# Kernel optimization log

Measured on AMD Instinct MI355X. Metric: run time of the kernel, lower is better.

Reference implementation:

```python
import jax, jax.numpy as jnp
import numpy as np

N = 50000
E = 1600000
EP = 500000
D_IN, D_EMB = 64, 32


def setup_inputs() -> dict:
    key = jax.random.key(0)
    ks = jax.random.split(key, 12)
    return {
        "x": jax.random.normal(ks[0], (N, D_IN), dtype=jnp.float32),
        "W1": jax.random.normal(ks[1], (D_IN, D_EMB), dtype=jnp.float32) * (1.0 / np.sqrt(D_IN)),
        "b1": jnp.zeros((D_EMB,), dtype=jnp.float32),
        "W2": jax.random.normal(ks[2], (D_EMB, 2 * D_EMB), dtype=jnp.float32) * (1.0 / np.sqrt(D_EMB)),
        "b2": jnp.zeros((2 * D_EMB,), dtype=jnp.float32),
        "eps": jax.random.normal(ks[3], (N, D_EMB), dtype=jnp.float32),
        "edge_src": jax.random.randint(ks[4], (E,), 0, N, dtype=jnp.int32),
        "edge_dst": jax.random.randint(ks[5], (E,), 0, N, dtype=jnp.int32),
        "pos_src": jax.random.randint(ks[6], (EP,), 0, N, dtype=jnp.int32),
        "pos_dst": jax.random.randint(ks[7], (EP,), 0, N, dtype=jnp.int32),
        "neg_src": jax.random.randint(ks[8], (EP,), 0, N, dtype=jnp.int32),
        "neg_dst": jax.random.randint(ks[9], (EP,), 0, N, dtype=jnp.int32),
    }


def _degree_norms(src, dst, n):
    ones = jnp.ones(src.shape, dtype=jnp.float32)
    out_deg = jax.ops.segment_sum(ones, src, num_segments=n)
    in_deg = jax.ops.segment_sum(ones, dst, num_segments=n)
    # DGL GraphConv norm='both': clamp degrees to >=1, pow(-0.5)
    return jnp.clip(out_deg, 1.0) ** -0.5, jnp.clip(in_deg, 1.0) ** -0.5


def _graph_conv(h, src, dst, norm_src, norm_dst, W, b, n):
    # rst = D_dst^{-1/2} A D_src^{-1/2} h W + b
    msg = (h * norm_src[:, None])[src]                       # [E, d] gather
    agg = jax.ops.segment_sum(msg, dst, num_segments=n)      # [N, d] scatter-add
    return (agg * norm_dst[:, None]) @ W + b


def _dot_predict(z, u, v):
    # u_dot_v: per-edge inner product of endpoint embeddings
    return jnp.sum(z[u] * z[v], axis=-1)


def reference(x, W1, b1, W2, b2, eps, edge_src, edge_dst,
              pos_src, pos_dst, neg_src, neg_dst):
    n = x.shape[0]
    ns, nd = _degree_norms(edge_src, edge_dst, n)
    h = _graph_conv(x, edge_src, edge_dst, ns, nd, W1, b1, n)
    h = jax.nn.relu(h)  # dropout = identity (eval mode)
    h = _graph_conv(h, edge_src, edge_dst, ns, nd, W2, b2, n)
    mu, log_var = jnp.split(h, 2, axis=-1)
    sigma = jnp.exp(log_var / 2.0)
    z = mu + sigma * eps
    pos = _dot_predict(z, pos_src, pos_dst)
    neg = _dot_predict(z, neg_src, neg_dst)
    return pos, neg, mu, sigma
```

## Files before the change

kernel.cpp:

```cpp
#include <hip/hip_runtime.h>
#include <math.h>

#define NN  50000
#define NE  1600000
#define NEP 500000
#define DIN 64
#define DE  32

#define BKT_SH 7
#define NB     391
#define S1B    250
#define CHK    6400
#define HB     128
#define HCHK   12500
#define HWRD   12500
#define XWB    3125

typedef float f4 __attribute__((ext_vector_type(4)));

__device__ __forceinline__ unsigned f2b(float f) {
    unsigned u = __float_as_uint(f);
    return (u + 0x7FFFu + ((u >> 16) & 1u)) >> 16;
}
__device__ __forceinline__ unsigned pack2(float a, float b) {
    return f2b(a) | (f2b(b) << 16);
}
__device__ __forceinline__ float blo(unsigned u) { return __uint_as_float(u << 16); }
__device__ __forceinline__ float bhi(unsigned u) { return __uint_as_float(u & 0xFFFF0000u); }

__global__ __launch_bounds__(256) void k_h1s1(const int* __restrict__ src,
                                              const int* __restrict__ dst,
                                              unsigned* __restrict__ partial,
                                              int* __restrict__ T) {
    __shared__ unsigned h[HWRD];
    int t = threadIdx.x;
    if (blockIdx.x < HB) {
        for (int i = t; i < HWRD; i += 256) h[i] = 0;
        __syncthreads();
        int beg = blockIdx.x * HCHK;
        const int ev = beg + HCHK;
        int i = beg + t;
        for (; i + 1792 < ev; i += 2048) {
            int s0 = src[i],        s1 = src[i + 256],  s2 = src[i + 512],  s3 = src[i + 768];
            int s4 = src[i + 1024], s5 = src[i + 1280], s6 = src[i + 1536], s7 = src[i + 1792];
            atomicAdd(&h[s0 >> 2], 1u << ((s0 & 3) * 8));
            atomicAdd(&h[s1 >> 2], 1u << ((s1 & 3) * 8));
            atomicAdd(&h[s2 >> 2], 1u << ((s2 & 3) * 8));
            atomicAdd(&h[s3 >> 2], 1u << ((s3 & 3) * 8));
            atomicAdd(&h[s4 >> 2], 1u << ((s4 & 3) * 8));
            atomicAdd(&h[s5 >> 2], 1u << ((s5 & 3) * 8));
            atomicAdd(&h[s6 >> 2], 1u << ((s6 & 3) * 8));
            atomicAdd(&h[s7 >> 2], 1u << ((s7 & 3) * 8));
        }
        for (; i < ev; i += 256) {
            int s = src[i];
            atomicAdd(&h[s >> 2], 1u << ((s & 3) * 8));
        }
        __syncthreads();
        unsigned* p = partial + (size_t)blockIdx.x * HWRD;
        for (int i2 = t; i2 < HWRD; i2 += 256) p[i2] = h[i2];
    } else {
        int b = blockIdx.x - HB;
        int* cd = (int*)h;
        for (int i = t; i < NB; i += 256) cd[i] = 0;
        __syncthreads();
        int beg = b * CHK;
        const int ev = beg + CHK;
        int i = beg + t;
        for (; i + 1792 < ev; i += 2048) {
            int d0 = dst[i],        d1 = dst[i + 256],  d2 = dst[i + 512],  d3 = dst[i + 768];
            int d4 = dst[i + 1024], d5 = dst[i + 1280], d6 = dst[i + 1536], d7 = dst[i + 1792];
            atomicAdd(&cd[d0 >> BKT_SH], 1);
            atomicAdd(&cd[d1 >> BKT_SH], 1);
            atomicAdd(&cd[d2 >> BKT_SH], 1);
            atomicAdd(&cd[d3 >> BKT_SH], 1);
            atomicAdd(&cd[d4 >> BKT_SH], 1);
            atomicAdd(&cd[d5 >> BKT_SH], 1);
            atomicAdd(&cd[d6 >> BKT_SH], 1);
            atomicAdd(&cd[d7 >> BKT_SH], 1);
        }
        for (; i < ev; i += 256)
            atomicAdd(&cd[dst[i] >> BKT_SH], 1);
        __syncthreads();
        for (int i2 = t; i2 < NB; i2 += 256) T[b * NB + i2] = cd[i2];
    }
}

__global__ __launch_bounds__(512) void k_s2h(const int* __restrict__ T,
                                             int* __restrict__ Base,
                                             int* __restrict__ BS,
                                             const unsigned* __restrict__ partial,
                                             int* __restrict__ degs) {
    int t = threadIdx.x;
    if (blockIdx.x == 0) {
        __shared__ int tot[512];
        int run = 0;
        if (t < NB) {
            for (int b = 0; b < S1B; b += 5) {
                int v0 = T[(b + 0) * NB + t];
                int v1 = T[(b + 1) * NB + t];
                int v2 = T[(b + 2) * NB + t];
                int v3 = T[(b + 3) * NB + t];
                int v4 = T[(b + 4) * NB + t];
                Base[(b + 0) * NB + t] = run; run += v0;
                Base[(b + 1) * NB + t] = run; run += v1;
                Base[(b + 2) * NB + t] = run; run += v2;
                Base[(b + 3) * NB + t] = run; run += v3;
                Base[(b + 4) * NB + t] = run; run += v4;
            }
        }
        tot[t] = (t < NB) ? run : 0;
        __syncthreads();
        for (int off = 1; off < 512; off <<= 1) {
            int v = (t >= off) ? tot[t - off] : 0;
            __syncthreads();
            tot[t] += v;
            __syncthreads();
        }
        if (t < NB) BS[t] = (t == 0) ? 0 : tot[t - 1];
        if (t == 0) BS[NB] = NE;
    } else {
        int w = (blockIdx.x - 1) * 512 + t;
        if (w < HWRD) {
            int c0 = 0, c1 = 0, c2 = 0, c3 = 0;
#pragma unroll 8
            for (int b = 0; b < HB; b++) {
                unsigned v = partial[(size_t)b * HWRD + w];
                c0 += (int)(v & 0xFFu);
                c1 += (int)((v >> 8) & 0xFFu);
                c2 += (int)((v >> 16) & 0xFFu);
                c3 += (int)(v >> 24);
            }
            ((int4*)degs)[w] = make_int4(c0, c1, c2, c3);
        }
    }
}

__global__ __launch_bounds__(512) void k_s3(const int* __restrict__ src,
                                            const int* __restrict__ dst,
                                            const int* __restrict__ T,
                                            const int* __restrict__ Base,
                                            const int* __restrict__ BS,
                                            unsigned* __restrict__ tmp) {
    __shared__ int scn[512];
    __shared__ int delta[NB];
    __shared__ int cur[NB];
    __shared__ unsigned buf[CHK];
    int t = threadIdx.x;
    int beg = blockIdx.x * CHK;
    scn[t] = (t < NB) ? T[blockIdx.x * NB + t] : 0;
    __syncthreads();
    for (int off = 1; off < 512; off <<= 1) {
        int v = (t >= off) ? scn[t - off] : 0;
        __syncthreads();
        scn[t] += v;
        __syncthreads();
    }
    if (t < NB) {
        int ls = (t == 0) ? 0 : scn[t - 1];
        cur[t] = ls;
        delta[t] = Base[blockIdx.x * NB + t] + BS[t] - ls;
    }
    __syncthreads();
    {
        const int ev = beg + CHK;
        int i = beg + t;
        for (; i + 1536 < ev; i += 2048) {
            int d0 = dst[i],        s0 = src[i];
            int d1 = dst[i + 512],  s1 = src[i + 512];
            int d2 = dst[i + 1024], s2 = src[i + 1024];
            int d3 = dst[i + 1536], s3 = src[i + 1536];
            int l0 = atomicAdd(&cur[d0 >> BKT_SH], 1); buf[l0] = (unsigned)s0 | ((unsigned)d0 << 16);
            int l1 = atomicAdd(&cur[d1 >> BKT_SH], 1); buf[l1] = (unsigned)s1 | ((unsigned)d1 << 16);
            int l2 = atomicAdd(&cur[d2 >> BKT_SH], 1); buf[l2] = (unsigned)s2 | ((unsigned)d2 << 16);
            int l3 = atomicAdd(&cur[d3 >> BKT_SH], 1); buf[l3] = (unsigned)s3 | ((unsigned)d3 << 16);
        }
        for (; i < ev; i += 512) {
            int d = dst[i];
            int s = src[i];
            int lp = atomicAdd(&cur[d >> BKT_SH], 1);
            buf[lp] = (unsigned)s | ((unsigned)d << 16);
        }
    }
    __syncthreads();
    for (int i = t; i < CHK; i += 512) {
        unsigned e = buf[i];
        tmp[delta[e >> (16 + BKT_SH)] + i] = e;
    }
}

__global__ __launch_bounds__(256) void k_s4x(const unsigned* __restrict__ tmp,
                                             const int* __restrict__ BS,
                                             ushort* __restrict__ csr,
                                             int* __restrict__ rowptr,
                                             const float* __restrict__ x,
                                             const float* __restrict__ W1,
                                             const int* __restrict__ degs,
                                             unsigned* __restrict__ xw1b) {
    __shared__ float sW[DIN * DE];
    int t = threadIdx.x;
    if (blockIdx.x < NB) {
        int* cnt = (int*)sW;
        int* scn = cnt + 128;
        int* cur = cnt + 256;
        int p = blockIdx.x;
        int ebeg = BS[p], eend = BS[p + 1];
        int ne = eend - ebeg;
        if (t < 128) cnt[t] = 0;
        __syncthreads();
        {
            int i = t;
            for (; i + 768 < ne; i += 1024) {
                unsigned e0 = tmp[ebeg + i];
                unsigned e1 = tmp[ebeg + i + 256];
                unsigned e2 = tmp[ebeg + i + 512];
                unsigned e3 = tmp[ebeg + i + 768];
                atomicAdd(&cnt[(e0 >> 16) & 127], 1);
                atomicAdd(&cnt[(e1 >> 16) & 127], 1);
                atomicAdd(&cnt[(e2 >> 16) & 127], 1);
                atomicAdd(&cnt[(e3 >> 16) & 127], 1);
            }
            for (; i < ne; i += 256)
                atomicAdd(&cnt[(tmp[ebeg + i] >> 16) & 127], 1);
        }
        __syncthreads();
        if (t < 128) scn[t] = cnt[t];
        __syncthreads();
        for (int off = 1; off < 128; off <<= 1) {
            int v = 0;
            if (t < 128 && t >= off) v = scn[t - off];
            __syncthreads();
            if (t < 128) scn[t] += v;
            __syncthreads();
        }
        if (t < 128) {
            int ex = (t == 0) ? 0 : scn[t - 1];
            cur[t] = ex;
            int node = (p << BKT_SH) + t;
            if (node < NN) rowptr[node] = ebeg + ex;
        }
        if (p == NB - 1 && t == 0) rowptr[NN] = NE;
        __syncthreads();
        {
            int i = t;
            for (; i + 768 < ne; i += 1024) {
                unsigned e0 = tmp[ebeg + i];
                unsigned e1 = tmp[ebeg + i + 256];
                unsigned e2 = tmp[ebeg + i + 512];
                unsigned e3 = tmp[ebeg + i + 768];
                int l0 = atomicAdd(&cur[(e0 >> 16) & 127], 1); csr[ebeg + l0] = (ushort)(e0 & 0xFFFFu);
                int l1 = atomicAdd(&cur[(e1 >> 16) & 127], 1); csr[ebeg + l1] = (ushort)(e1 & 0xFFFFu);
                int l2 = atomicAdd(&cur[(e2 >> 16) & 127], 1); csr[ebeg + l2] = (ushort)(e2 & 0xFFFFu);
                int l3 = atomicAdd(&cur[(e3 >> 16) & 127], 1); csr[ebeg + l3] = (ushort)(e3 & 0xFFFFu);
            }
            for (; i < ne; i += 256) {
                unsigned e = tmp[ebeg + i];
                int lp = atomicAdd(&cur[(e >> 16) & 127], 1);
                csr[ebeg + lp] = (ushort)(e & 0xFFFFu);
            }
        }
    } else {
        for (int i = t; i < DIN * DE; i += 256) sW[i] = W1[i];
        __syncthreads();
        int r  = (blockIdx.x - NB) * 16 + (t >> 4);
        int tc = t & 15;
        const float* xr = x + (size_t)r * DIN;
        float a0 = 0.f, a1 = 0.f;
#pragma unroll
        for (int k = 0; k < DIN; k++) {
            float v = xr[k];
            a0 += v * sW[k * DE + 2 * tc];
            a1 += v * sW[k * DE + 2 * tc + 1];
        }
        float ns = rsqrtf(fmaxf((float)degs[r], 1.0f));
        xw1b[r * 16 + tc] = pack2(a0 * ns, a1 * ns);
    }
}

__device__ __forceinline__ void acc8(float* a, uint4 w) {
    a[0] += blo(w.x); a[1] += bhi(w.x);
    a[2] += blo(w.y); a[3] += bhi(w.y);
    a[4] += blo(w.z); a[5] += bhi(w.z);
    a[6] += blo(w.w); a[7] += bhi(w.w);
}

__device__ __forceinline__ void gather_q(const ushort* __restrict__ crow,
                                         const uint4* __restrict__ msg,
                                         int len, int h, int l, float* a) {
    int n8 = len >> 3;
    for (int b = h; b < n8; b += 4) {
        const ushort* p = crow + b * 8;
        int s0 = p[0], s1 = p[1], s2 = p[2], s3 = p[3];
        int s4 = p[4], s5 = p[5], s6 = p[6], s7 = p[7];
        uint4 w0 = msg[s0 * 4 + l];
        uint4 w1 = msg[s1 * 4 + l];
        uint4 w2 = msg[s2 * 4 + l];
        uint4 w3 = msg[s3 * 4 + l];
        uint4 w4 = msg[s4 * 4 + l];
        uint4 w5 = msg[s5 * 4 + l];
        uint4 w6 = msg[s6 * 4 + l];
        uint4 w7 = msg[s7 * 4 + l];
        acc8(a, w0); acc8(a, w1); acc8(a, w2); acc8(a, w3);
        acc8(a, w4); acc8(a, w5); acc8(a, w6); acc8(a, w7);
    }
    int tail = len & 7;
    if (tail && h == (n8 & 3)) {
        const ushort* p = crow + n8 * 8;
        for (int k = 0; k < tail; k++) {
            uint4 w = msg[(int)p[k] * 4 + l];
            acc8(a, w);
        }
    }
}

__global__ __launch_bounds__(256) void k_g1(const int* __restrict__ rowptr,
                                            const ushort* __restrict__ csr,
                                            const uint4* __restrict__ msg,
                                            const int* __restrict__ degs,
                                            const float* __restrict__ b1,
                                            uint4* __restrict__ out) {
    int t = blockIdx.x * 256 + threadIdx.x;
    int r = t >> 4;
    int l = t & 3;
    int h = (t >> 2) & 3;
    if (r >= NN) return;
    int beg = rowptr[r];
    int end = rowptr[r + 1];
    int len = end - beg;
    float a[8] = {0, 0, 0, 0, 0, 0, 0, 0};
    gather_q(csr + beg, msg, len, h, l, a);
#pragma unroll
    for (int k = 0; k < 8; k++) a[k] += __shfl_xor(a[k], 4);
#pragma unroll
    for (int k = 0; k < 8; k++) a[k] += __shfl_xor(a[k], 8);
    if (h) return;
    float scd = rsqrtf(fmaxf((float)len, 1.0f));
    float scs = rsqrtf(fmaxf((float)degs[r], 1.0f));
    const float4* b14 = (const float4*)b1;
    float4 bb0 = b14[2 * l], bb1 = b14[2 * l + 1];
    float o0 = fmaxf(scd * a[0] + bb0.x, 0.f) * scs;
    float o1 = fmaxf(scd * a[1] + bb0.y, 0.f) * scs;
    float o2 = fmaxf(scd * a[2] + bb0.z, 0.f) * scs;
    float o3 = fmaxf(scd * a[3] + bb0.w, 0.f) * scs;
    float o4 = fmaxf(scd * a[4] + bb1.x, 0.f) * scs;
    float o5 = fmaxf(scd * a[5] + bb1.y, 0.f) * scs;
    float o6 = fmaxf(scd * a[6] + bb1.z, 0.f) * scs;
    float o7 = fmaxf(scd * a[7] + bb1.w, 0.f) * scs;
    out[r * 4 + l] = make_uint4(pack2(o0, o1), pack2(o2, o3), pack2(o4, o5), pack2(o6, o7));
}

__global__ __launch_bounds__(256) void k_g2f(const int* __restrict__ rowptr,
                                             const ushort* __restrict__ csr,
                                             const uint4* __restrict__ msg,
                                             const float* __restrict__ W2,
                                             const float* __restrict__ b2,
                                             const float* __restrict__ eps,
                                             float* __restrict__ mu,
                                             float* __restrict__ sigma,
                                             unsigned* __restrict__ zb) {
    __shared__ float sW[DE * 64];
    __shared__ float sb[64];
    int t = threadIdx.x;
    for (int i = t; i < DE * 64; i += 256) sW[i] = W2[i];
    if (t < 64) sb[t] = b2[t];
    __syncthreads();
    int g = blockIdx.x * 256 + t;
    int r = g >> 4;
    int l = g & 3;
    int j = g & 15;
    int h = (g >> 2) & 3;
    if (r >= NN) return;
    int beg = rowptr[r];
    int end = rowptr[r + 1];
    int len = end - beg;
    float a[8] = {0, 0, 0, 0, 0, 0, 0, 0};
    gather_q(csr + beg, msg, len, h, l, a);
#pragma unroll
    for (int k = 0; k < 8; k++) a[k] += __shfl_xor(a[k], 4);
#pragma unroll
    for (int k = 0; k < 8; k++) a[k] += __shfl_xor(a[k], 8);
    float scd = rsqrtf(fmaxf((float)len, 1.0f));
#pragma unroll
    for (int k = 0; k < 8; k++) a[k] *= scd;
    int cbase = 4 * j;
    float o3[4];
#pragma unroll
    for (int c = 0; c < 4; c++) o3[c] = sb[cbase + c];
#pragma unroll
    for (int d = 0; d < 4; d++) {
        int kb = 8 * (l ^ d);
#pragma unroll
        for (int k = 0; k < 8; k++) {
            float av = (d == 0) ? a[k] : __shfl_xor(a[k], d);
            const float* wrow = sW + (kb + k) * 64 + cbase;
#pragma unroll
            for (int c = 0; c < 4; c++) o3[c] += av * wrow[c];
        }
    }
    if (j < 8) {
        f4* mp = (f4*)(mu + (size_t)r * DE + cbase);
        f4 m0 = {o3[0], o3[1], o3[2], o3[3]};
        __builtin_nontemporal_store(m0, mp);
    }
    float muv[4];
#pragma unroll
    for (int c = 0; c < 4; c++) muv[c] = __shfl_xor(o3[c], 8);
    if (j >= 8) {
        int cc = cbase - DE;
        const f4* ep = (const f4*)(eps + (size_t)r * DE + cc);
        f4 e0 = __builtin_nontemporal_load(ep);
        float ev[4] = {e0.x, e0.y, e0.z, e0.w};
        float sgv[4], zv[4];
#pragma unroll
        for (int c = 0; c < 4; c++) {
            sgv[c] = expf(0.5f * o3[c]);
            zv[c]  = muv[c] + sgv[c] * ev[c];
        }
        f4* sp = (f4*)(sigma + (size_t)r * DE + cc);
        f4 s0 = {sgv[0], sgv[1], sgv[2], sgv[3]};
        __builtin_nontemporal_store(s0, sp);
        uint2* zp = (uint2*)(zb + (size_t)r * 16 + (j - 8) * 2);
        *zp = make_uint2(pack2(zv[0], zv[1]), pack2(zv[2], zv[3]));
    }
}

__global__ __launch_bounds__(256) void k_dot2(const uint4* __restrict__ zb4,
                                              const int* __restrict__ pu,
                                              const int* __restrict__ pv,
                                              const int* __restrict__ nu,
                                              const int* __restrict__ nv,
                                              float* __restrict__ out) {
    int t = blockIdx.x * 256 + threadIdx.x;
    int e = t >> 2;
    int l = t & 3;
    if (e < 2 * NEP) {
        int ee = (e < NEP) ? e : e - NEP;
        const int* uu = (e < NEP) ? pu : nu;
        const int* vv = (e < NEP) ? pv : nv;
        int a = __builtin_nontemporal_load(uu + ee);
        int b = __builtin_nontemporal_load(vv + ee);
        uint4 za = zb4[a * 4 + l];
        uint4 zc = zb4[b * 4 + l];
        float s = blo(za.x) * blo(zc.x) + bhi(za.x) * bhi(zc.x)
                + blo(za.y) * blo(zc.y) + bhi(za.y) * bhi(zc.y)
                + blo(za.z) * blo(zc.z) + bhi(za.z) * bhi(zc.z)
                + blo(za.w) * blo(zc.w) + bhi(za.w) * bhi(zc.w);
        s += __shfl_xor(s, 1);
        s += __shfl_xor(s, 2);
        if (l == 0) __builtin_nontemporal_store(s, out + e);
    }
}

extern "C" void kernel_launch(void* const* d_in, const int* in_sizes, int n_in,
                              void* d_out, int out_size, void* d_ws, size_t ws_size,
                              hipStream_t stream) {
    const float* x    = (const float*)d_in[0];
    const float* W1   = (const float*)d_in[1];
    const float* b1   = (const float*)d_in[2];
    const float* W2   = (const float*)d_in[3];
    const float* b2   = (const float*)d_in[4];
    const float* eps  = (const float*)d_in[5];
    const int*   esrc = (const int*)d_in[6];
    const int*   edst = (const int*)d_in[7];
    const int*   psrc = (const int*)d_in[8];
    const int*   pdst = (const int*)d_in[9];
    const int*   gsrc = (const int*)d_in[10];
    const int*   gdst = (const int*)d_in[11];

    float* out = (float*)d_out;
    float* pos = out;
    float* mu  = out + 2 * NEP;
    float* sg  = out + 2 * NEP + NN * DE;

    int* wi = (int*)d_ws;
    int*      rowptr  = wi;
    int*      T       = wi + 50001;
    int*      Base    = wi + 147751;
    int*      BS      = wi + 245501;
    int*      degs    = wi + 245896;
    ushort*   csr     = (ushort*)(wi + 295896);
    unsigned* partial = (unsigned*)(wi + 1895896);
    unsigned* tmp     = (unsigned*)(wi + 3495896);
    unsigned* P0      = (unsigned*)(wi + 5095896);
    unsigned* P1      = P0 + 16 * NN;

    k_h1s1<<<HB + S1B, 256, 0, stream>>>(esrc, edst, partial, T);
    k_s2h <<<1 + (HWRD + 511) / 512, 512, 0, stream>>>(T, Base, BS, partial, degs);
    k_s3  <<<S1B, 512, 0, stream>>>(esrc, edst, T, Base, BS, tmp);
    k_s4x <<<NB + XWB, 256, 0, stream>>>(tmp, BS, csr, rowptr, x, W1, degs, P0);
    k_g1  <<<(NN * 16 + 255) / 256, 256, 0, stream>>>(rowptr, csr, (const uint4*)P0, degs, b1, (uint4*)P1);
    k_g2f <<<(NN * 16 + 255) / 256, 256, 0, stream>>>(rowptr, csr, (const uint4*)P1, W2, b2, eps, mu, sg, P0);
    k_dot2<<<(2 * NEP * 4) / 256, 256, 0, stream>>>((const uint4*)P0, psrc, pdst, gsrc, gdst, pos);
}
```

Before: 211.0 us.

## Replace per-node CSR build with bucket-local LDS atomic aggregation

Drops the second sorting pass that built a per-node CSR and rowptr. Both graph-conv layers now aggregate directly from the bucket-sorted edge list, one block per 128-node destination bucket, using float atomics on a padded shared-memory accumulator. In-degree is counted in that same loop. The x·W1 projection is merged into the bucket-scatter kernel, and the layer-2 dense transform now runs 4 lanes per node with 16 outputs each. This saves one kernel launch and a full pass over the edges. The cost is heavy LDS atomic contention and a summation order that is no longer deterministic, and only 391 blocks are launched for the aggregation.

```diff
diff --git a/kernel.cpp b/kernel.cpp
--- a/kernel.cpp
+++ b/kernel.cpp
@@ -14,7 +14,7 @@
 #define HB     128
 #define HCHK   12500
 #define HWRD   12500
-#define XWB    3125
+#define XWB    1563
 
 typedef float f4 __attribute__((ext_vector_type(4)));
 
@@ -90,7 +90,7 @@
                                              int* __restrict__ Base,
                                              int* __restrict__ BS,
                                              const unsigned* __restrict__ partial,
-                                             int* __restrict__ degs) {
+                                             int* __restrict__ dout) {
     int t = threadIdx.x;
     if (blockIdx.x == 0) {
         __shared__ int tot[512];
@@ -131,139 +131,74 @@
                 c2 += (int)((v >> 16) & 0xFFu);
                 c3 += (int)(v >> 24);
             }
-            ((int4*)degs)[w] = make_int4(c0, c1, c2, c3);
-        }
-    }
-}
-
-__global__ __launch_bounds__(512) void k_s3(const int* __restrict__ src,
-                                            const int* __restrict__ dst,
-                                            const int* __restrict__ T,
-                                            const int* __restrict__ Base,
-                                            const int* __restrict__ BS,
-                                            unsigned* __restrict__ tmp) {
+            ((int4*)dout)[w] = make_int4(c0, c1, c2, c3);
+        }
+    }
+}
+
+__global__ __launch_bounds__(512) void k_s3x(const int* __restrict__ src,
+                                             const int* __restrict__ dst,
+                                             const int* __restrict__ T,
+                                             const int* __restrict__ Base,
+                                             const int* __restrict__ BS,
+                                             unsigned* __restrict__ tmp,
+                                             const float* __restrict__ x,
+                                             const float* __restrict__ W1,
+                                             const int* __restrict__ dout,
+                                             unsigned* __restrict__ xw1b) {
     __shared__ int scn[512];
     __shared__ int delta[NB];
     __shared__ int cur[NB];
     __shared__ unsigned buf[CHK];
     int t = threadIdx.x;
-    int beg = blockIdx.x * CHK;
-    scn[t] = (t < NB) ? T[blockIdx.x * NB + t] : 0;
-    __syncthreads();
-    for (int off = 1; off < 512; off <<= 1) {
-        int v = (t >= off) ? scn[t - off] : 0;
-        __syncthreads();
-        scn[t] += v;
-        __syncthreads();
-    }
-    if (t < NB) {
-        int ls = (t == 0) ? 0 : scn[t - 1];
-        cur[t] = ls;
-        delta[t] = Base[blockIdx.x * NB + t] + BS[t] - ls;
-    }
-    __syncthreads();
-    {
-        const int ev = beg + CHK;
-        int i = beg + t;
-        for (; i + 1536 < ev; i += 2048) {
-            int d0 = dst[i],        s0 = src[i];
-            int d1 = dst[i + 512],  s1 = src[i + 512];
-            int d2 = dst[i + 1024], s2 = src[i + 1024];
-            int d3 = dst[i + 1536], s3 = src[i + 1536];
-            int l0 = atomicAdd(&cur[d0 >> BKT_SH], 1); buf[l0] = (unsigned)s0 | ((unsigned)d0 << 16);
-            int l1 = atomicAdd(&cur[d1 >> BKT_SH], 1); buf[l1] = (unsigned)s1 | ((unsigned)d1 << 16);
-            int l2 = atomicAdd(&cur[d2 >> BKT_SH], 1); buf[l2] = (unsigned)s2 | ((unsigned)d2 << 16);
-            int l3 = atomicAdd(&cur[d3 >> BKT_SH], 1); buf[l3] = (unsigned)s3 | ((unsigned)d3 << 16);
-        }
-        for (; i < ev; i += 512) {
-            int d = dst[i];
-            int s = src[i];
-            int lp = atomicAdd(&cur[d >> BKT_SH], 1);
-            buf[lp] = (unsigned)s | ((unsigned)d << 16);
-        }
-    }
-    __syncthreads();
-    for (int i = t; i < CHK; i += 512) {
-        unsigned e = buf[i];
-        tmp[delta[e >> (16 + BKT_SH)] + i] = e;
-    }
-}
-
-__global__ __launch_bounds__(256) void k_s4x(const unsigned* __restrict__ tmp,
-                                             const int* __restrict__ BS,
-                                             ushort* __restrict__ csr,
-                                             int* __restrict__ rowptr,
-                                             const float* __restrict__ x,
-                                             const float* __restrict__ W1,
-                                             const int* __restrict__ degs,
-                                             unsigned* __restrict__ xw1b) {
-    __shared__ float sW[DIN * DE];
-    int t = threadIdx.x;
-    if (blockIdx.x < NB) {
-        int* cnt = (int*)sW;
-        int* scn = cnt + 128;
-        int* cur = cnt + 256;
-        int p = blockIdx.x;
-        int ebeg = BS[p], eend = BS[p + 1];
-        int ne = eend - ebeg;
-        if (t < 128) cnt[t] = 0;
+    if (blockIdx.x < S1B) {
+        int beg = blockIdx.x * CHK;
+        scn[t] = (t < NB) ? T[blockIdx.x * NB + t] : 0;
+        __syncthreads();
+        for (int off = 1; off < 512; off <<= 1) {
+            int v = (t >= off) ? scn[t - off] : 0;
+            __syncthreads();
+            scn[t] += v;
+            __syncthreads();
+        }
+        if (t < NB) {
+            int ls = (t == 0) ? 0 : scn[t - 1];
+            cur[t] = ls;
+            delta[t] = Base[blockIdx.x * NB + t] + BS[t] - ls;
+        }
         __syncthreads();
         {
-            int i = t;
-            for (; i + 768 < ne; i += 1024) {
-                unsigned e0 = tmp[ebeg + i];
-                unsigned e1 = tmp[ebeg + i + 256];
-                unsigned e2 = tmp[ebeg + i + 512];
-                unsigned e3 = tmp[ebeg + i + 768];
-                atomicAdd(&cnt[(e0 >> 16) & 127], 1);
-                atomicAdd(&cnt[(e1 >> 16) & 127], 1);
-                atomicAdd(&cnt[(e2 >> 16) & 127], 1);
-                atomicAdd(&cnt[(e3 >> 16) & 127], 1);
+            const int ev = beg + CHK;
+            int i = beg + t;
+            for (; i + 1536 < ev; i += 2048) {
+                int d0 = dst[i],        s0 = src[i];
+                int d1 = dst[i + 512],  s1 = src[i + 512];
+                int d2 = dst[i + 1024], s2 = src[i + 1024];
+                int d3 = dst[i + 1536], s3 = src[i + 1536];
+                int l0 = atomicAdd(&cur[d0 >> BKT_SH], 1); buf[l0] = (unsigned)s0 | ((unsigned)d0 << 16);
+                int l1 = atomicAdd(&cur[d1 >> BKT_SH], 1); buf[l1] = (unsigned)s1 | ((unsigned)d1 << 16);
+                int l2 = atomicAdd(&cur[d2 >> BKT_SH], 1); buf[l2] = (unsigned)s2 | ((unsigned)d2 << 16);
+                int l3 = atomicAdd(&cur[d3 >> BKT_SH], 1); buf[l3] = (unsigned)s3 | ((unsigned)d3 << 16);
             }
-            for (; i < ne; i += 256)
-                atomicAdd(&cnt[(tmp[ebeg + i] >> 16) & 127], 1);
-        }
-        __syncthreads();
-        if (t < 128) scn[t] = cnt[t];
-        __syncthreads();
-        for (int off = 1; off < 128; off <<= 1) {
-            int v = 0;
-            if (t < 128 && t >= off) v = scn[t - off];
-            __syncthreads();
-            if (t < 128) scn[t] += v;
-            __syncthreads();
-        }
-        if (t < 128) {
-            int ex = (t == 0) ? 0 : scn[t - 1];
-            cur[t] = ex;
-            int node = (p << BKT_SH) + t;
-            if (node < NN) rowptr[node] = ebeg + ex;
-        }
-        if (p == NB - 1 && t == 0) rowptr[NN] = NE;
-        __syncthreads();
-        {
-            int i = t;
-            for (; i + 768 < ne; i += 1024) {
-                unsigned e0 = tmp[ebeg + i];
-                unsigned e1 = tmp[ebeg + i + 256];
-                unsigned e2 = tmp[ebeg + i + 512];
-                unsigned e3 = tmp[ebeg + i + 768];
-                int l0 = atomicAdd(&cur[(e0 >> 16) & 127], 1); csr[ebeg + l0] = (ushort)(e0 & 0xFFFFu);
-                int l1 = atomicAdd(&cur[(e1 >> 16) & 127], 1); csr[ebeg + l1] = (ushort)(e1 & 0xFFFFu);
-                int l2 = atomicAdd(&cur[(e2 >> 16) & 127], 1); csr[ebeg + l2] = (ushort)(e2 & 0xFFFFu);
-                int l3 = atomicAdd(&cur[(e3 >> 16) & 127], 1); csr[ebeg + l3] = (ushort)(e3 & 0xFFFFu);
+            for (; i < ev; i += 512) {
+                int d = dst[i];
+                int s = src[i];
+                int lp = atomicAdd(&cur[d >> BKT_SH], 1);
+                buf[lp] = (unsigned)s | ((unsigned)d << 16);
             }
-            for (; i < ne; i += 256) {
-                unsigned e = tmp[ebeg + i];
-                int lp = atomicAdd(&cur[(e >> 16) & 127], 1);
-                csr[ebeg + lp] = (ushort)(e & 0xFFFFu);
-            }
+        }
+        __syncthreads();
+        for (int i = t; i < CHK; i += 512) {
+            unsigned e = buf[i];
+            tmp[delta[e >> (16 + BKT_SH)] + i] = e;
         }
     } else {
-        for (int i = t; i < DIN * DE; i += 256) sW[i] = W1[i];
-        __syncthreads();
-        int r  = (blockIdx.x - NB) * 16 + (t >> 4);
+        float* sW = (float*)buf;
+        for (int i = t; i < DIN * DE; i += 512) sW[i] = W1[i];
+        __syncthreads();
+        int r  = (blockIdx.x - S1B) * 32 + (t >> 4);
         int tc = t & 15;
+        if (r >= NN) return;
         const float* xr = x + (size_t)r * DIN;
         float a0 = 0.f, a1 = 0.f;
 #pragma unroll
@@ -272,155 +207,231 @@
             a0 += v * sW[k * DE + 2 * tc];
             a1 += v * sW[k * DE + 2 * tc + 1];
         }
-        float ns = rsqrtf(fmaxf((float)degs[r], 1.0f));
+        float ns = rsqrtf(fmaxf((float)dout[r], 1.0f));
         xw1b[r * 16 + tc] = pack2(a0 * ns, a1 * ns);
     }
 }
 
-__device__ __forceinline__ void acc8(float* a, uint4 w) {
-    a[0] += blo(w.x); a[1] += bhi(w.x);
-    a[2] += blo(w.y); a[3] += bhi(w.y);
-    a[4] += blo(w.z); a[5] += bhi(w.z);
-    a[6] += blo(w.w); a[7] += bhi(w.w);
-}
-
-__device__ __forceinline__ void gather_q(const ushort* __restrict__ crow,
-                                         const uint4* __restrict__ msg,
-                                         int len, int h, int l, float* a) {
-    int n8 = len >> 3;
-    for (int b = h; b < n8; b += 4) {
-        const ushort* p = crow + b * 8;
-        int s0 = p[0], s1 = p[1], s2 = p[2], s3 = p[3];
-        int s4 = p[4], s5 = p[5], s6 = p[6], s7 = p[7];
-        uint4 w0 = msg[s0 * 4 + l];
-        uint4 w1 = msg[s1 * 4 + l];
-        uint4 w2 = msg[s2 * 4 + l];
-        uint4 w3 = msg[s3 * 4 + l];
-        uint4 w4 = msg[s4 * 4 + l];
-        uint4 w5 = msg[s5 * 4 + l];
-        uint4 w6 = msg[s6 * 4 + l];
-        uint4 w7 = msg[s7 * 4 + l];
-        acc8(a, w0); acc8(a, w1); acc8(a, w2); acc8(a, w3);
-        acc8(a, w4); acc8(a, w5); acc8(a, w6); acc8(a, w7);
-    }
-    int tail = len & 7;
-    if (tail && h == (n8 & 3)) {
-        const ushort* p = crow + n8 * 8;
-        for (int k = 0; k < tail; k++) {
-            uint4 w = msg[(int)p[k] * 4 + l];
-            acc8(a, w);
-        }
-    }
-}
-
-__global__ __launch_bounds__(256) void k_g1(const int* __restrict__ rowptr,
-                                            const ushort* __restrict__ csr,
-                                            const uint4* __restrict__ msg,
-                                            const int* __restrict__ degs,
-                                            const float* __restrict__ b1,
-                                            uint4* __restrict__ out) {
-    int t = blockIdx.x * 256 + threadIdx.x;
-    int r = t >> 4;
+__global__ __launch_bounds__(512) void k_agg1(const unsigned* __restrict__ tmp,
+                                              const int* __restrict__ BS,
+                                              const uint4* __restrict__ msg,
+                                              const int* __restrict__ dout,
+                                              const float* __restrict__ b1,
+                                              uint4* __restrict__ out) {
+    __shared__ float agg[128 * 33];
+    __shared__ int cnt[128];
+    __shared__ float sb1[DE];
+    int t = threadIdx.x;
+    int p = blockIdx.x;
+    for (int i = t; i < 128 * 33; i += 512) agg[i] = 0.f;
+    if (t < 128) cnt[t] = 0;
+    if (t < DE) sb1[t] = b1[t];
+    __syncthreads();
+    int ebeg = BS[p];
+    int ne = BS[p + 1] - ebeg;
     int l = t & 3;
-    int h = (t >> 2) & 3;
-    if (r >= NN) return;
-    int beg = rowptr[r];
-    int end = rowptr[r + 1];
-    int len = end - beg;
-    float a[8] = {0, 0, 0, 0, 0, 0, 0, 0};
-    gather_q(csr + beg, msg, len, h, l, a);
-#pragma unroll
-    for (int k = 0; k < 8; k++) a[k] += __shfl_xor(a[k], 4);
-#pragma unroll
-    for (int k = 0; k < 8; k++) a[k] += __shfl_xor(a[k], 8);
-    if (h) return;
-    float scd = rsqrtf(fmaxf((float)len, 1.0f));
-    float scs = rsqrtf(fmaxf((float)degs[r], 1.0f));
-    const float4* b14 = (const float4*)b1;
-    float4 bb0 = b14[2 * l], bb1 = b14[2 * l + 1];
-    float o0 = fmaxf(scd * a[0] + bb0.x, 0.f) * scs;
-    float o1 = fmaxf(scd * a[1] + bb0.y, 0.f) * scs;
-    float o2 = fmaxf(scd * a[2] + bb0.z, 0.f) * scs;
-    float o3 = fmaxf(scd * a[3] + bb0.w, 0.f) * scs;
-    float o4 = fmaxf(scd * a[4] + bb1.x, 0.f) * scs;
-    float o5 = fmaxf(scd * a[5] + bb1.y, 0.f) * scs;
-    float o6 = fmaxf(scd * a[6] + bb1.z, 0.f) * scs;
-    float o7 = fmaxf(scd * a[7] + bb1.w, 0.f) * scs;
-    out[r * 4 + l] = make_uint4(pack2(o0, o1), pack2(o2, o3), pack2(o4, o5), pack2(o6, o7));
-}
-
-__global__ __launch_bounds__(256) void k_g2f(const int* __restrict__ rowptr,
-                                             const ushort* __restrict__ csr,
-                                             const uint4* __restrict__ msg,
-                                             const float* __restrict__ W2,
-                                             const float* __restrict__ b2,
-                                             const float* __restrict__ eps,
-                                             float* __restrict__ mu,
-                                             float* __restrict__ sigma,
-                                             unsigned* __restrict__ zb) {
+    int base = t >> 2;
+    int i = base;
+    for (; i + 384 < ne; i += 512) {
+        unsigned e0 = tmp[ebeg + i];
+        unsigned e1 = tmp[ebeg + i + 128];
+        unsigned e2 = tmp[ebeg + i + 256];
+        unsigned e3 = tmp[ebeg + i + 384];
+        uint4 w0 = msg[(e0 & 0xFFFFu) * 4 + l];
+        uint4 w1 = msg[(e1 & 0xFFFFu) * 4 + l];
+        uint4 w2 = msg[(e2 & 0xFFFFu) * 4 + l];
+        uint4 w3 = msg[(e3 & 0xFFFFu) * 4 + l];
+        int d0 = (e0 >> 16) & 127, d1 = (e1 >> 16) & 127;
+        int d2 = (e2 >> 16) & 127, d3 = (e3 >> 16) & 127;
+        if (l == 0) {
+            atomicAdd(&cnt[d0], 1); atomicAdd(&cnt[d1], 1);
+            atomicAdd(&cnt[d2], 1); atomicAdd(&cnt[d3], 1);
+        }
+        float* a0 = agg + d0 * 33 + l * 8;
+        float* a1 = agg + d1 * 33 + l * 8;
+        float* a2 = agg + d2 * 33 + l * 8;
+        float* a3 = agg + d3 * 33 + l * 8;
+        atomicAdd(a0 + 0, blo(w0.x)); atomicAdd(a0 + 1, bhi(w0.x));
+        atomicAdd(a0 + 2, blo(w0.y)); atomicAdd(a0 + 3, bhi(w0.y));
+        atomicAdd(a0 + 4, blo(w0.z)); atomicAdd(a0 + 5, bhi(w0.z));
+        atomicAdd(a0 + 6, blo(w0.w)); atomicAdd(a0 + 7, bhi(w0.w));
+        atomicAdd(a1 + 0, blo(w1.x)); atomicAdd(a1 + 1, bhi(w1.x));
+        atomicAdd(a1 + 2, blo(w1.y)); atomicAdd(a1 + 3, bhi(w1.y));
+        atomicAdd(a1 + 4, blo(w1.z)); atomicAdd(a1 + 5, bhi(w1.z));
+        atomicAdd(a1 + 6, blo(w1.w)); atomicAdd(a1 + 7, bhi(w1.w));
+        atomicAdd(a2 + 0, blo(w2.x)); atomicAdd(a2 + 1, bhi(w2.x));
+        atomicAdd(a2 + 2, blo(w2.y)); atomicAdd(a2 + 3, bhi(w2.y));
+        atomicAdd(a2 + 4, blo(w2.z)); atomicAdd(a2 + 5, bhi(w2.z));
+        atomicAdd(a2 + 6, blo(w2.w)); atomicAdd(a2 + 7, bhi(w2.w));
+        atomicAdd(a3 + 0, blo(w3.x)); atomicAdd(a3 + 1, bhi(w3.x));
+        atomicAdd(a3 + 2, blo(w3.y)); atomicAdd(a3 + 3, bhi(w3.y));
+        atomicAdd(a3 + 4, blo(w3.z)); atomicAdd(a3 + 5, bhi(w3.z));
+        atomicAdd(a3 + 6, blo(w3.w)); atomicAdd(a3 + 7, bhi(w3.w));
+    }
+    for (; i < ne; i += 128) {
+        unsigned e = tmp[ebeg + i];
+        uint4 w = msg[(e & 0xFFFFu) * 4 + l];
+        int d = (e >> 16) & 127;
+        if (l == 0) atomicAdd(&cnt[d], 1);
+        float* a = agg + d * 33 + l * 8;
+        atomicAdd(a + 0, blo(w.x)); atomicAdd(a + 1, bhi(w.x));
+        atomicAdd(a + 2, blo(w.y)); atomicAdd(a + 3, bhi(w.y));
+        atomicAdd(a + 4, blo(w.z)); atomicAdd(a + 5, bhi(w.z));
+        atomicAdd(a + 6, blo(w.w)); atomicAdd(a + 7, bhi(w.w));
+    }
+    __syncthreads();
+    int n = t >> 2;
+    int node = (p << BKT_SH) + n;
+    if (node < NN) {
+        float scd = rsqrtf(fmaxf((float)cnt[n], 1.0f));
+        float scs = rsqrtf(fmaxf((float)dout[node], 1.0f));
+        const float* a = agg + n * 33 + l * 8;
+        float o0 = fmaxf(scd * a[0] + sb1[l * 8 + 0], 0.f) * scs;
+        float o1 = fmaxf(scd * a[1] + sb1[l * 8 + 1], 0.f) * scs;
+        float o2 = fmaxf(scd * a[2] + sb1[l * 8 + 2], 0.f) * scs;
+        float o3 = fmaxf(scd * a[3] + sb1[l * 8 + 3], 0.f) * scs;
+        float o4 = fmaxf(scd * a[4] + sb1[l * 8 + 4], 0.f) * scs;
+        float o5 = fmaxf(scd * a[5] + sb1[l * 8 + 5], 0.f) * scs;
+        float o6 = fmaxf(scd * a[6] + sb1[l * 8 + 6], 0.f) * scs;
+        float o7 = fmaxf(scd * a[7] + sb1[l * 8 + 7], 0.f) * scs;
+        out[node * 4 + l] = make_uint4(pack2(o0, o1), pack2(o2, o3), pack2(o4, o5), pack2(o6, o7));
+    }
+}
+
+__global__ __launch_bounds__(512) void k_agg2(const unsigned* __restrict__ tmp,
+                                              const int* __restrict__ BS,
+                                              const uint4* __restrict__ msg,
+                                              const float* __restrict__ W2,
+                                              const float* __restrict__ b2,
+                                              const float* __restrict__ eps,
+                                              float* __restrict__ mu,
+                                              float* __restrict__ sigma,
+                                              unsigned* __restrict__ zb) {
+    __shared__ float agg[128 * 33];
+    __shared__ int cnt[128];
     __shared__ float sW[DE * 64];
     __shared__ float sb[64];
     int t = threadIdx.x;
-    for (int i = t; i < DE * 64; i += 256) sW[i] = W2[i];
+    int p = blockIdx.x;
+    for (int i = t; i < 128 * 33; i += 512) agg[i] = 0.f;
+    if (t < 128) cnt[t] = 0;
+    for (int i = t; i < DE * 64; i += 512) sW[i] = W2[i];
     if (t < 64) sb[t] = b2[t];
     __syncthreads();
-    int g = blockIdx.x * 256 + t;
-    int r = g >> 4;
-    int l = g & 3;
-    int j = g & 15;
-    int h = (g >> 2) & 3;
-    if (r >= NN) return;
-    int beg = rowptr[r];
-    int end = rowptr[r + 1];
-    int len = end - beg;
-    float a[8] = {0, 0, 0, 0, 0, 0, 0, 0};
-    gather_q(csr + beg, msg, len, h, l, a);
-#pragma unroll
-    for (int k = 0; k < 8; k++) a[k] += __shfl_xor(a[k], 4);
-#pragma unroll
-    for (int k = 0; k < 8; k++) a[k] += __shfl_xor(a[k], 8);
-    float scd = rsqrtf(fmaxf((float)len, 1.0f));
-#pragma unroll
-    for (int k = 0; k < 8; k++) a[k] *= scd;
-    int cbase = 4 * j;
-    float o3[4];
-#pragma unroll
-    for (int c = 0; c < 4; c++) o3[c] = sb[cbase + c];
-#pragma unroll
-    for (int d = 0; d < 4; d++) {
-        int kb = 8 * (l ^ d);
-#pragma unroll
-        for (int k = 0; k < 8; k++) {
-            float av = (d == 0) ? a[k] : __shfl_xor(a[k], d);
-            const float* wrow = sW + (kb + k) * 64 + cbase;
-#pragma unroll
-            for (int c = 0; c < 4; c++) o3[c] += av * wrow[c];
-        }
-    }
-    if (j < 8) {
-        f4* mp = (f4*)(mu + (size_t)r * DE + cbase);
-        f4 m0 = {o3[0], o3[1], o3[2], o3[3]};
+    int ebeg = BS[p];
+    int ne = BS[p + 1] - ebeg;
+    int l = t & 3;
+    int base = t >> 2;
+    int i = base;
+    for (; i + 384 < ne; i += 512) {
+        unsigned e0 = tmp[ebeg + i];
+        unsigned e1 = tmp[ebeg + i + 128];
+        unsigned e2 = tmp[ebeg + i + 256];
+        unsigned e3 = tmp[ebeg + i + 384];
+        uint4 w0 = msg[(e0 & 0xFFFFu) * 4 + l];
+        uint4 w1 = msg[(e1 & 0xFFFFu) * 4 + l];
+        uint4 w2 = msg[(e2 & 0xFFFFu) * 4 + l];
+        uint4 w3 = msg[(e3 & 0xFFFFu) * 4 + l];
+        int d0 = (e0 >> 16) & 127, d1 = (e1 >> 16) & 127;
+        int d2 = (e2 >> 16) & 127, d3 = (e3 >> 16) & 127;
+        if (l == 0) {
+            atomicAdd(&cnt[d0], 1); atomicAdd(&cnt[d1], 1);
+            atomicAdd(&cnt[d2], 1); atomicAdd(&cnt[d3], 1);
+        }
+        float* a0 = agg + d0 * 33 + l * 8;
+        float* a1 = agg + d1 * 33 + l * 8;
+        float* a2 = agg + d2 * 33 + l * 8;
+        float* a3 = agg + d3 * 33 + l * 8;
+        atomicAdd(a0 + 0, blo(w0.x)); atomicAdd(a0 + 1, bhi(w0.x));
+        atomicAdd(a0 + 2, blo(w0.y)); atomicAdd(a0 + 3, bhi(w0.y));
+        atomicAdd(a0 + 4, blo(w0.z)); atomicAdd(a0 + 5, bhi(w0.z));
+        atomicAdd(a0 + 6, blo(w0.w)); atomicAdd(a0 + 7, bhi(w0.w));
+        atomicAdd(a1 + 0, blo(w1.x)); atomicAdd(a1 + 1, bhi(w1.x));
+        atomicAdd(a1 + 2, blo(w1.y)); atomicAdd(a1 + 3, bhi(w1.y));
+        atomicAdd(a1 + 4, blo(w1.z)); atomicAdd(a1 + 5, bhi(w1.z));
+        atomicAdd(a1 + 6, blo(w1.w)); atomicAdd(a1 + 7, bhi(w1.w));
+        atomicAdd(a2 + 0, blo(w2.x)); atomicAdd(a2 + 1, bhi(w2.x));
+        atomicAdd(a2 + 2, blo(w2.y)); atomicAdd(a2 + 3, bhi(w2.y));
+        atomicAdd(a2 + 4, blo(w2.z)); atomicAdd(a2 + 5, bhi(w2.z));
+        atomicAdd(a2 + 6, blo(w2.w)); atomicAdd(a2 + 7, bhi(w2.w));
+        atomicAdd(a3 + 0, blo(w3.x)); atomicAdd(a3 + 1, bhi(w3.x));
+        atomicAdd(a3 + 2, blo(w3.y)); atomicAdd(a3 + 3, bhi(w3.y));
+        atomicAdd(a3 + 4, blo(w3.z)); atomicAdd(a3 + 5, bhi(w3.z));
+        atomicAdd(a3 + 6, blo(w3.w)); atomicAdd(a3 + 7, bhi(w3.w));
+    }
+    for (; i < ne; i += 128) {
+        unsigned e = tmp[ebeg + i];
+        uint4 w = msg[(e & 0xFFFFu) * 4 + l];
+        int d = (e >> 16) & 127;
+        if (l == 0) atomicAdd(&cnt[d], 1);
+        float* a = agg + d * 33 + l * 8;
+        atomicAdd(a + 0, blo(w.x)); atomicAdd(a + 1, bhi(w.x));
+        atomicAdd(a + 2, blo(w.y)); atomicAdd(a + 3, bhi(w.y));
+        atomicAdd(a + 4, blo(w.z)); atomicAdd(a + 5, bhi(w.z));
+        atomicAdd(a + 6, blo(w.w)); atomicAdd(a + 7, bhi(w.w));
+    }
+    __syncthreads();
+    int n = t >> 2;
+    int node = (p << BKT_SH) + n;
+    if (node >= NN) return;
+    float scd = rsqrtf(fmaxf((float)cnt[n], 1.0f));
+    float a[DE];
+#pragma unroll
+    for (int k = 0; k < DE; k++) a[k] = agg[n * 33 + k] * scd;
+    int cb = 16 * l;
+    float o[16];
+#pragma unroll
+    for (int c = 0; c < 16; c++) o[c] = sb[cb + c];
+#pragma unroll
+    for (int k = 0; k < DE; k++) {
+        float av = a[k];
+        const float* wr = sW + k * 64 + cb;
+#pragma unroll
+        for (int c = 0; c < 16; c++) o[c] += av * wr[c];
+    }
+    if (l < 2) {
+        f4* mp = (f4*)(mu + (size_t)node * DE + cb);
+        f4 m0 = {o[0],  o[1],  o[2],  o[3]};
+        f4 m1 = {o[4],  o[5],  o[6],  o[7]};
+        f4 m2 = {o[8],  o[9],  o[10], o[11]};
+        f4 m3 = {o[12], o[13], o[14], o[15]};
         __builtin_nontemporal_store(m0, mp);
-    }
-    float muv[4];
-#pragma unroll
-    for (int c = 0; c < 4; c++) muv[c] = __shfl_xor(o3[c], 8);
-    if (j >= 8) {
-        int cc = cbase - DE;
-        const f4* ep = (const f4*)(eps + (size_t)r * DE + cc);
+        __builtin_nontemporal_store(m1, mp + 1);
+        __builtin_nontemporal_store(m2, mp + 2);
+        __builtin_nontemporal_store(m3, mp + 3);
+    }
+    float muv[16];
+#pragma unroll
+    for (int c = 0; c < 16; c++) muv[c] = __shfl_xor(o[c], 2);
+    if (l >= 2) {
+        int cc = cb - DE;
+        const f4* ep = (const f4*)(eps + (size_t)node * DE + cc);
         f4 e0 = __builtin_nontemporal_load(ep);
-        float ev[4] = {e0.x, e0.y, e0.z, e0.w};
-        float sgv[4], zv[4];
-#pragma unroll
-        for (int c = 0; c < 4; c++) {
-            sgv[c] = expf(0.5f * o3[c]);
+        f4 e1 = __builtin_nontemporal_load(ep + 1);
+        f4 e2 = __builtin_nontemporal_load(ep + 2);
+        f4 e3 = __builtin_nontemporal_load(ep + 3);
+        float ev[16] = {e0.x, e0.y, e0.z, e0.w, e1.x, e1.y, e1.z, e1.w,
+                        e2.x, e2.y, e2.z, e2.w, e3.x, e3.y, e3.z, e3.w};
+        float sgv[16], zv[16];
+#pragma unroll
+        for (int c = 0; c < 16; c++) {
+            sgv[c] = expf(0.5f * o[c]);
             zv[c]  = muv[c] + sgv[c] * ev[c];
         }
-        f4* sp = (f4*)(sigma + (size_t)r * DE + cc);
-        f4 s0 = {sgv[0], sgv[1], sgv[2], sgv[3]};
+        f4* sp = (f4*)(sigma + (size_t)node * DE + cc);
+        f4 s0 = {sgv[0],  sgv[1],  sgv[2],  sgv[3]};
+        f4 s1 = {sgv[4],  sgv[5],  sgv[6],  sgv[7]};
+        f4 s2 = {sgv[8],  sgv[9],  sgv[10], sgv[11]};
+        f4 s3 = {sgv[12], sgv[13], sgv[14], sgv[15]};
         __builtin_nontemporal_store(s0, sp);
-        uint2* zp = (uint2*)(zb + (size_t)r * 16 + (j - 8) * 2);
-        *zp = make_uint2(pack2(zv[0], zv[1]), pack2(zv[2], zv[3]));
+        __builtin_nontemporal_store(s1, sp + 1);
+        __builtin_nontemporal_store(s2, sp + 2);
+        __builtin_nontemporal_store(s3, sp + 3);
+        uint4* zp = (uint4*)(zb + (size_t)node * 16 + (l - 2) * 8);
+        zp[0] = make_uint4(pack2(zv[0],  zv[1]),  pack2(zv[2],  zv[3]),
+                           pack2(zv[4],  zv[5]),  pack2(zv[6],  zv[7]));
+        zp[1] = make_uint4(pack2(zv[8],  zv[9]),  pack2(zv[10], zv[11]),
+                           pack2(zv[12], zv[13]), pack2(zv[14], zv[15]));
     }
 }
 
@@ -473,22 +484,19 @@
     float* sg  = out + 2 * NEP + NN * DE;
 
     int* wi = (int*)d_ws;
-    int*      rowptr  = wi;
-    int*      T       = wi + 50001;
-    int*      Base    = wi + 147751;
-    int*      BS      = wi + 245501;
-    int*      degs    = wi + 245896;
-    ushort*   csr     = (ushort*)(wi + 295896);
-    unsigned* partial = (unsigned*)(wi + 1895896);
-    unsigned* tmp     = (unsigned*)(wi + 3495896);
-    unsigned* P0      = (unsigned*)(wi + 5095896);
+    int*      dout_   = wi;
+    int*      T       = wi + 50000;
+    int*      Base    = wi + 147750;
+    int*      BS      = wi + 245500;
+    unsigned* partial = (unsigned*)(wi + 245900);
+    unsigned* tmp     = (unsigned*)(wi + 1845900);
+    unsigned* P0      = (unsigned*)(wi + 3445900);
     unsigned* P1      = P0 + 16 * NN;
 
     k_h1s1<<<HB + S1B, 256, 0, stream>>>(esrc, edst, partial, T);
-    k_s2h <<<1 + (HWRD + 511) / 512, 512, 0, stream>>>(T, Base, BS, partial, degs);
-    k_s3  <<<S1B, 512, 0, stream>>>(esrc, edst, T, Base, BS, tmp);
-    k_s4x <<<NB + XWB, 256, 0, stream>>>(tmp, BS, csr, rowptr, x, W1, degs, P0);
-    k_g1  <<<(NN * 16 + 255) / 256, 256, 0, stream>>>(rowptr, csr, (const uint4*)P0, degs, b1, (uint4*)P1);
-    k_g2f <<<(NN * 16 + 255) / 256, 256, 0, stream>>>(rowptr, csr, (const uint4*)P1, W2, b2, eps, mu, sg, P0);
+    k_s2h <<<26, 512, 0, stream>>>(T, Base, BS, partial, dout_);
+    k_s3x <<<S1B + XWB, 512, 0, stream>>>(esrc, edst, T, Base, BS, tmp, x, W1, dout_, P0);
+    k_agg1<<<NB, 512, 0, stream>>>(tmp, BS, (const uint4*)P0, dout_, b1, (uint4*)P1);
+    k_agg2<<<NB, 512, 0, stream>>>(tmp, BS, (const uint4*)P1, W2, b2, eps, mu, sg, P0);
     k_dot2<<<(2 * NEP * 4) / 256, 256, 0, stream>>>((const uint4*)P0, psrc, pdst, gsrc, gdst, pos);
 }
```

Measured after the change: 839.2 us. 3.98x slower.
